# Kernel optimization log

Measured on AMD Instinct MI355X. Metric: run time of the kernel, lower is better.

The kernel has to match this reference:

```python
import jax, jax.numpy as jnp
import numpy as np

K = 3            # kernel size
C_IN = 8
C_OUT = 16
PATCH = C_IN * K * K  # 72
EPS = 1e-6


def setup_inputs() -> dict:
    key = jax.random.key(0)
    k1, k2, k3 = jax.random.split(key, 3)
    in_tensor = jax.random.normal(k1, (4, C_IN, 112, 112), dtype=jnp.float32)
    # 1x1-conv weighting predictor: C_in -> PATCH*C_OUT channels
    w_pred = jax.random.normal(k2, (PATCH * C_OUT, C_IN), dtype=jnp.float32) * 0.05
    b_pred = jax.random.normal(k3, (PATCH * C_OUT,), dtype=jnp.float32) * 0.05
    return {"in_tensor": in_tensor, "w_pred": w_pred, "b_pred": b_pred}


def reference(in_tensor, w_pred, b_pred):
    B, C, H, W = in_tensor.shape
    # --- weighting module: predict dynamic weights per spatial location ---
    raw = jnp.einsum('bchw,oc->bohw', in_tensor, w_pred) + b_pred[None, :, None, None]
    weightings = raw.reshape(B, PATCH, C_OUT, H, W)          # [B, C*k*k, C_out, H, W]
    # norm = L2 norm of the dynamic weight over the patch dim -> [B, C_out, H, W]
    norm = jnp.sqrt(jnp.sum(weightings * weightings, axis=1)) + EPS
    # --- unfold: overlapping k x k patches, same padding, stride 1 ---
    patches = jax.lax.conv_general_dilated_patches(
        in_tensor, (K, K), (1, 1), 'SAME')                   # [B, C*k*k, H, W]
    # --- weighted sum over the patch dim, then normalize ---
    activations = jnp.einsum('bphw,bpohw->bohw', patches, weightings)  # [B, C_out, H, W]
    return activations / norm
```

## Files before the change

### kernel.cpp

```cpp
#include <hip/hip_runtime.h>
#include <math.h>

#define IMG_W 112
#define HW    12544
#define CI    8
#define CO    16
#define NP    72
#define EPS   1e-6f

typedef __attribute__((ext_vector_type(8))) short short8;
typedef __attribute__((ext_vector_type(4))) float f32x4;

static __device__ inline short f2bf(float f) {
  unsigned u = __float_as_uint(f);
  return (short)((u + 0x7FFFu + ((u >> 16) & 1u)) >> 16);
}

static constexpr int DQ[9] = {-113, -112, -111, -1, 0, 1, 111, 112, 113};

__global__ __launch_bounds__(512) void coda_mfma(
    const float* __restrict__ in, const float* __restrict__ wp,
    const float* __restrict__ bp, float* __restrict__ out)
{
  __shared__ short sA[NP][32][8];
  __shared__ float sBuf[CI * 290];
  __shared__ short sZ[16];

  const int tid = threadIdx.x;
  const int b   = blockIdx.x / 196;
  const int r0  = (blockIdx.x - b * 196) * 64;
  const float* __restrict__ inb = in + b * CI * HW;

  for (int idx = tid; idx < NP * 32; idx += 512) {
    const int p = idx >> 5, l = idx & 31, q = l >> 4, m = l & 15;
    const int row = p * 16 + m;
    short8 v = {0, 0, 0, 0, 0, 0, 0, 0};
    if (q == 0) {
      const float* wr = wp + row * CI;
#pragma unroll
      for (int j = 0; j < 8; ++j) v[j] = f2bf(wr[j]);
    } else {
      v[0] = f2bf(bp[row]);
    }
    *(short8*)&sA[p][l][0] = v;
  }
  if (tid < 16) sZ[tid] = 0;
  for (int k = tid; k < CI * 290; k += 512) {
    const int c = k / 290;
    const int i = k - c * 290;
    int gg = r0 - 113 + i;
    gg = (gg < 0) ? 0 : (gg > HW - 1 ? HW - 1 : gg);
    sBuf[k] = inb[c * HW + gg];
  }
  __syncthreads();

  const int wave = tid >> 6;
  const int lane = tid & 63;
  const int g    = wave & 3;
  const int half = wave >> 2;
  const int ln   = lane & 15;
  const int quad = lane >> 4;
  const int rwav = r0 + g * 16;
  const int h    = rwav / IMG_W;
  const int wl   = (rwav - h * IMG_W) + ln;
  const int off  = g * 16 + ln + 113;

  float vm[9];
#pragma unroll
  for (int q = 0; q < 9; ++q) {
    const int kh = q / 3, kw = q % 3;
    const bool ok = ((unsigned)(h + kh - 1) < 112u) &&
                    ((unsigned)(wl + kw - 1) < 112u);
    vm[q] = ok ? 1.f : 0.f;
  }

  short8 bf = {0, 0, 0, 0, 0, 0, 0, 0};
#pragma unroll
  for (int j = 0; j < 8; ++j) {
    const short bv = f2bf(sBuf[j * 290 + off]);
    bf[j] = (quad == 0) ? bv : ((quad == 1 && j == 0) ? (short)0x3F80 : (short)0);
  }

  float acc[4] = {0.f, 0.f, 0.f, 0.f};
  float n2[4]  = {0.f, 0.f, 0.f, 0.f};
  const bool qlo = (quad < 2);
  const int  c0  = half * 4;

#pragma unroll
  for (int cc = 0; cc < 4; ++cc) {
    const int c = c0 + cc;
    const float* __restrict__ sc = &sBuf[c * 290 + off];
#pragma unroll
    for (int q = 0; q < 9; ++q) {
      const int p = c * 9 + q;
      const short* ap = qlo ? &sA[p][quad * 16 + ln][0] : &sZ[0];
      const short8 af = *(const short8*)ap;
      const float pv = vm[q] * sc[DQ[q]];
      const f32x4 zc = {0.f, 0.f, 0.f, 0.f};
      const f32x4 d = __builtin_amdgcn_mfma_f32_16x16x32_bf16(af, bf, zc, 0, 0, 0);
#pragma unroll
      for (int i = 0; i < 4; ++i) {
        acc[i] = fmaf(pv, d[i], acc[i]);
        n2[i]  = fmaf(d[i], d[i], n2[i]);
      }
    }
  }

  __syncthreads();
  if (half == 1) {
#pragma unroll
    for (int i = 0; i < 4; ++i) {
      sBuf[i * 256 + g * 64 + lane]       = acc[i];
      sBuf[(i + 4) * 256 + g * 64 + lane] = n2[i];
    }
  }
  __syncthreads();
  if (half == 0) {
    float* __restrict__ ob = out + (long)b * CO * HW + rwav + ln;
#pragma unroll
    for (int i = 0; i < 4; ++i) {
      const float a2 = acc[i] + sBuf[i * 256 + g * 64 + lane];
      const float s2 = n2[i] + sBuf[(i + 4) * 256 + g * 64 + lane];
      const int co = quad * 4 + i;
      ob[(long)co * HW] = a2 / (sqrtf(s2) + EPS);
    }
  }
}

extern "C" void kernel_launch(void* const* d_in, const int* in_sizes, int n_in,
                              void* d_out, int out_size, void* d_ws, size_t ws_size,
                              hipStream_t stream) {
  const float* in = (const float*)d_in[0];
  const float* wp = (const float*)d_in[1];
  const float* bp = (const float*)d_in[2];
  float* out = (float*)d_out;

  coda_mfma<<<dim3(784), dim3(512), 0, stream>>>(in, wp, bp, out);
}
```

Measured before the change: 72.22 us.

## Switch to 32x32x16 MFMA packing two patch positions per instruction

Replaces the 16x16x32 bf16 MFMA, which wasted half its K dimension and half its A rows on zero padding, with a 32x32x16 MFMA. Each instruction now computes two patch positions, giving 32 output rows, using K=8 weights plus a bias slot. This halves the MFMA count per channel group. The block shrinks to 256 threads with four waves covering 64 pixels, and the A tile layout and output lane mapping change to match. Occupancy is hinted at 3 blocks per SM. The cost is more accumulator registers and a larger per-wave epilogue.

Result: slower. 77.09 us (+6.7%).

```diff
diff --git a/kernel.cpp b/kernel.cpp
--- a/kernel.cpp
+++ b/kernel.cpp
@@ -5,11 +5,11 @@
 #define HW    12544
 #define CI    8
 #define CO    16
-#define NP    72
+#define NP2   36
 #define EPS   1e-6f
 
 typedef __attribute__((ext_vector_type(8))) short short8;
-typedef __attribute__((ext_vector_type(4))) float f32x4;
+typedef __attribute__((ext_vector_type(16))) float f32x16;
 
 static __device__ inline short f2bf(float f) {
   unsigned u = __float_as_uint(f);
@@ -18,34 +18,32 @@
 
 static constexpr int DQ[9] = {-113, -112, -111, -1, 0, 1, 111, 112, 113};
 
-__global__ __launch_bounds__(512) void coda_mfma(
+__global__ __launch_bounds__(256, 3) void coda_mfma(
     const float* __restrict__ in, const float* __restrict__ wp,
     const float* __restrict__ bp, float* __restrict__ out)
 {
-  __shared__ short sA[NP][32][8];
+  __shared__ short sA[NP2][2][32][8];
   __shared__ float sBuf[CI * 290];
-  __shared__ short sZ[16];
 
   const int tid = threadIdx.x;
   const int b   = blockIdx.x / 196;
   const int r0  = (blockIdx.x - b * 196) * 64;
   const float* __restrict__ inb = in + b * CI * HW;
 
-  for (int idx = tid; idx < NP * 32; idx += 512) {
-    const int p = idx >> 5, l = idx & 31, q = l >> 4, m = l & 15;
-    const int row = p * 16 + m;
+  for (int idx = tid; idx < NP2 * 64; idx += 256) {
+    const int p2 = idx >> 6, l = idx & 63, ah = l >> 5, m = l & 31;
+    const int row = p2 * 32 + m;
     short8 v = {0, 0, 0, 0, 0, 0, 0, 0};
-    if (q == 0) {
+    if (ah == 0) {
       const float* wr = wp + row * CI;
 #pragma unroll
       for (int j = 0; j < 8; ++j) v[j] = f2bf(wr[j]);
     } else {
       v[0] = f2bf(bp[row]);
     }
-    *(short8*)&sA[p][l][0] = v;
+    *(short8*)&sA[p2][ah][m][0] = v;
   }
-  if (tid < 16) sZ[tid] = 0;
-  for (int k = tid; k < CI * 290; k += 512) {
+  for (int k = tid; k < CI * 290; k += 256) {
     const int c = k / 290;
     const int i = k - c * 290;
     int gg = r0 - 113 + i;
@@ -56,72 +54,73 @@
 
   const int wave = tid >> 6;
   const int lane = tid & 63;
-  const int g    = wave & 3;
-  const int half = wave >> 2;
-  const int ln   = lane & 15;
-  const int quad = lane >> 4;
-  const int rwav = r0 + g * 16;
-  const int h    = rwav / IMG_W;
-  const int wl   = (rwav - h * IMG_W) + ln;
-  const int off  = g * 16 + ln + 113;
+  const int g    = wave & 1;
+  const int hh   = wave >> 1;
+  const int ln   = lane & 31;
+  const int hi   = lane >> 5;
+  const int px   = r0 + g * 32 + ln;
+  const int hrow = px / IMG_W;
+  const int wcol = px - hrow * IMG_W;
+  const int off  = g * 32 + ln + 113;
 
   float vm[9];
 #pragma unroll
   for (int q = 0; q < 9; ++q) {
     const int kh = q / 3, kw = q % 3;
-    const bool ok = ((unsigned)(h + kh - 1) < 112u) &&
-                    ((unsigned)(wl + kw - 1) < 112u);
+    const bool ok = ((unsigned)(hrow + kh - 1) < 112u) &&
+                    ((unsigned)(wcol + kw - 1) < 112u);
     vm[q] = ok ? 1.f : 0.f;
   }
 
-  short8 bf = {0, 0, 0, 0, 0, 0, 0, 0};
+  short8 bf;
 #pragma unroll
   for (int j = 0; j < 8; ++j) {
     const short bv = f2bf(sBuf[j * 290 + off]);
-    bf[j] = (quad == 0) ? bv : ((quad == 1 && j == 0) ? (short)0x3F80 : (short)0);
+    bf[j] = (hi == 0) ? bv : ((j == 0) ? (short)0x3F80 : (short)0);
   }
 
-  float acc[4] = {0.f, 0.f, 0.f, 0.f};
-  float n2[4]  = {0.f, 0.f, 0.f, 0.f};
-  const bool qlo = (quad < 2);
-  const int  c0  = half * 4;
+  float acc[8] = {0.f, 0.f, 0.f, 0.f, 0.f, 0.f, 0.f, 0.f};
+  float n2[8]  = {0.f, 0.f, 0.f, 0.f, 0.f, 0.f, 0.f, 0.f};
 
 #pragma unroll
-  for (int cc = 0; cc < 4; ++cc) {
-    const int c = c0 + cc;
-    const float* __restrict__ sc = &sBuf[c * 290 + off];
+  for (int t = 0; t < 18; ++t) {
+    const int c0_ = 4 * hh + (2 * t) / 9;
+    const int q0_ = (2 * t) % 9;
+    const int c1_ = 4 * hh + (2 * t + 1) / 9;
+    const int q1_ = (2 * t + 1) % 9;
+
+    const short8 af = *(const short8*)&sA[hh * 18 + t][hi][ln][0];
+    const float pv0 = vm[q0_] * sBuf[c0_ * 290 + off + DQ[q0_]];
+    const float pv1 = vm[q1_] * sBuf[c1_ * 290 + off + DQ[q1_]];
+
+    const f32x16 zc = {0.f, 0.f, 0.f, 0.f, 0.f, 0.f, 0.f, 0.f,
+                       0.f, 0.f, 0.f, 0.f, 0.f, 0.f, 0.f, 0.f};
+    const f32x16 d =
+        __builtin_amdgcn_mfma_f32_32x32x16_bf16(af, bf, zc, 0, 0, 0);
 #pragma unroll
-    for (int q = 0; q < 9; ++q) {
-      const int p = c * 9 + q;
-      const short* ap = qlo ? &sA[p][quad * 16 + ln][0] : &sZ[0];
-      const short8 af = *(const short8*)ap;
-      const float pv = vm[q] * sc[DQ[q]];
-      const f32x4 zc = {0.f, 0.f, 0.f, 0.f};
-      const f32x4 d = __builtin_amdgcn_mfma_f32_16x16x32_bf16(af, bf, zc, 0, 0, 0);
-#pragma unroll
-      for (int i = 0; i < 4; ++i) {
-        acc[i] = fmaf(pv, d[i], acc[i]);
-        n2[i]  = fmaf(d[i], d[i], n2[i]);
-      }
+    for (int i = 0; i < 16; ++i) {
+      const float pv = (i < 8) ? pv0 : pv1;
+      acc[i & 7] = fmaf(pv, d[i], acc[i & 7]);
+      n2[i & 7]  = fmaf(d[i], d[i], n2[i & 7]);
     }
   }
 
   __syncthreads();
-  if (half == 1) {
+  if (hh == 1) {
 #pragma unroll
-    for (int i = 0; i < 4; ++i) {
-      sBuf[i * 256 + g * 64 + lane]       = acc[i];
-      sBuf[(i + 4) * 256 + g * 64 + lane] = n2[i];
+    for (int j = 0; j < 8; ++j) {
+      sBuf[j * 128 + g * 64 + lane]       = acc[j];
+      sBuf[(j + 8) * 128 + g * 64 + lane] = n2[j];
     }
   }
   __syncthreads();
-  if (half == 0) {
-    float* __restrict__ ob = out + (long)b * CO * HW + rwav + ln;
+  if (hh == 0) {
+    float* __restrict__ ob = out + (long)b * CO * HW + px;
 #pragma unroll
-    for (int i = 0; i < 4; ++i) {
-      const float a2 = acc[i] + sBuf[i * 256 + g * 64 + lane];
-      const float s2 = n2[i] + sBuf[(i + 4) * 256 + g * 64 + lane];
-      const int co = quad * 4 + i;
+    for (int j = 0; j < 8; ++j) {
+      const float a2 = acc[j] + sBuf[j * 128 + g * 64 + lane];
+      const float s2 = n2[j] + sBuf[(j + 8) * 128 + g * 64 + lane];
+      const int co = (j & 3) + 8 * (j >> 2) + 4 * hi;
       ob[(long)co * HW] = a2 / (sqrtf(s2) + EPS);
     }
   }
@@ -135,5 +134,5 @@
   const float* bp = (const float*)d_in[2];
   float* out = (float*)d_out;
 
-  coda_mfma<<<dim3(784), dim3(512), 0, stream>>>(in, wp, bp, out);
+  coda_mfma<<<dim3(784), dim3(256), 0, stream>>>(in, wp, bp, out);
 }
```
